# Performance work log

Hardware: AMD Instinct MI355X
Metric: run time of the kernel (lower is better)

Reference implementation:

```python
import jax, jax.numpy as jnp
import numpy as np

N, C, H, W, D = 4, 320, 16, 16, 16
POS_RATIO = 0.5


def setup_inputs() -> dict:
    key = jax.random.key(0)
    k1, k2, k3, k4 = jax.random.split(key, 4)
    q = jax.random.normal(k1, (N, C, H, W, D), jnp.float32)
    k = jax.random.normal(k2, (N, C, H, W, D), jnp.float32)

    def make_coord(kr):
        # crop boxes: upper-left corner in [0, 0.4), extent in [0.4, 0.6)
        start = jax.random.uniform(kr, (N, 3), jnp.float32) * 0.4
        size = 0.4 + jax.random.uniform(jax.random.fold_in(kr, 1), (N, 3), jnp.float32) * 0.2
        return jnp.concatenate([start, start + size], axis=1)  # (N, 6)

    coord_q = make_coord(k3)
    coord_k = make_coord(k4)
    return {"q": q, "k": k, "coord_q": coord_q, "coord_k": coord_k}


def _centers(coord, h, w, d):
    """coord: (N,6) -> centers (N, h*w*d, 3) of each voxel in global coords, and bin diag (N,)."""
    dims = jnp.array([h, w, d], jnp.float32)
    bin_sz = (coord[:, 3:6] - coord[:, 0:3]) / dims  # (N,3) = (bin_h, bin_w, bin_d)
    ax = jnp.arange(h, dtype=jnp.float32) + 0.5
    ay = jnp.arange(w, dtype=jnp.float32) + 0.5
    az = jnp.arange(d, dtype=jnp.float32) + 0.5
    grid = jnp.stack(jnp.meshgrid(ax, ay, az, indexing="ij"), axis=-1)  # (h,w,d,3)
    grid = grid.reshape(1, h * w * d, 3)
    centers = grid * bin_sz[:, None, :] + coord[:, None, 0:3]  # (N, L, 3)
    diag = jnp.sqrt(jnp.sum(bin_sz ** 2, axis=-1))  # (N,)
    return centers, diag


def reference(q, k, coord_q, coord_k):
    n, c, h, w, d = q.shape
    L = h * w * d
    qf = q.reshape(n, c, L)
    kf = k.reshape(n, c, L)

    cq, diag_q = _centers(coord_q, h, w, d)  # (N,L,3), (N,)
    ck, diag_k = _centers(coord_k, h, w, d)
    max_diag = jnp.maximum(diag_q, diag_k)[:, None, None]  # (N,1,1)

    def masked_loss(q_flat, centers_q):
        # pairwise center distance (N, L, L) -- sum of three squared diffs, no (N,L,L,3) stack
        d2 = ((centers_q[:, :, None, 0] - ck[:, None, :, 0]) ** 2
              + (centers_q[:, :, None, 1] - ck[:, None, :, 1]) ** 2
              + (centers_q[:, :, None, 2] - ck[:, None, :, 2]) ** 2)
        dist = jnp.sqrt(d2) / max_diag
        mask = jax.lax.stop_gradient((dist < POS_RATIO).astype(jnp.float32))
        logit = jnp.einsum("ncl,ncm->nlm", q_flat, kf)  # bmm(q^T, k)
        return jnp.sum(logit * mask, axis=(-2, -1)) / (jnp.sum(mask, axis=(-2, -1)) + 1e-6)

    loss = masked_loss(qf, cq)
    # anatomy branch: flip(q) and flipped q-centers along batch dim 0 (as in source flip(x, dim=0))
    loss_rev = masked_loss(jnp.flip(qf, axis=0), jnp.flip(cq, axis=0))
    return -2.0 * jnp.mean(loss) - 2.0 * jnp.mean(loss_rev)
```

## Files before the change

kernel.cpp:

```cpp
#include <hip/hip_runtime.h>

#define LVOX   4096
#define NCH    320
#define NCOMBO 8
#define RCAP   49152

struct Geo {
    float qs0, qs1, qs2, qo0, qo1, qo2;
    float ks0, ks1, ks2, ko0, ko1, ko2;
    float ik0, ik1, ik2;
    float T;
};

__device__ __forceinline__ Geo make_geo(const float* __restrict__ cq,
                                        const float* __restrict__ ck,
                                        int n, int qb) {
    Geo g;
    const float* qc = cq + qb * 6;
    const float* qn = cq + n * 6;
    const float* kc = ck + n * 6;
    g.qs0 = (qc[3] - qc[0]) * (1.f / 16.f); g.qo0 = qc[0];
    g.qs1 = (qc[4] - qc[1]) * (1.f / 16.f); g.qo1 = qc[1];
    g.qs2 = (qc[5] - qc[2]) * (1.f / 16.f); g.qo2 = qc[2];
    g.ks0 = (kc[3] - kc[0]) * (1.f / 16.f); g.ko0 = kc[0];
    g.ks1 = (kc[4] - kc[1]) * (1.f / 16.f); g.ko1 = kc[1];
    g.ks2 = (kc[5] - kc[2]) * (1.f / 16.f); g.ko2 = kc[2];
    g.ik0 = 1.f / g.ks0; g.ik1 = 1.f / g.ks1; g.ik2 = 1.f / g.ks2;
    float b0 = (qn[3] - qn[0]) * (1.f / 16.f);
    float b1 = (qn[4] - qn[1]) * (1.f / 16.f);
    float b2 = (qn[5] - qn[2]) * (1.f / 16.f);
    float dq = sqrtf(b0 * b0 + b1 * b1 + b2 * b2);
    float dk = sqrtf(g.ks0 * g.ks0 + g.ks1 * g.ks1 + g.ks2 * g.ks2);
    g.T = 0.5f * fmaxf(dq, dk);
    return g;
}

__device__ __forceinline__ void axrange(float c, float ko, float ik, float T,
                                        int& m0, int& m1) {
    float lo = (c - T - ko) * ik - 0.5f;
    float hi = (c + T - ko) * ik - 0.5f;
    m0 = max((int)ceilf(lo) - 1, 0);
    m1 = min((int)floorf(hi) + 1, 15);
}

__global__ void enum_runs(const float* __restrict__ coord_q,
                          const float* __restrict__ coord_k,
                          unsigned* __restrict__ pcnt,
                          unsigned* __restrict__ rcnt,
                          unsigned* __restrict__ runs, int cap) {
    int gid = blockIdx.x * 256 + threadIdx.x;
    int j = gid >> 12;
    int l = gid & 4095;
    int n = j & 3;
    int qb = (j & 4) ? (3 - n) : n;
    Geo g = make_geo(coord_q, coord_k, n, qb);

    int ix = l >> 8, iy = (l >> 4) & 15, iz = l & 15;
    float cx = (ix + 0.5f) * g.qs0 + g.qo0;
    float cy = (iy + 0.5f) * g.qs1 + g.qo1;
    float cz = (iz + 0.5f) * g.qs2 + g.qo2;
    int x0, x1, y0, y1, z0, z1;
    axrange(cx, g.ko0, g.ik0, g.T, x0, x1);
    axrange(cy, g.ko1, g.ik1, g.T, y0, y1);
    axrange(cz, g.ko2, g.ik2, g.T, z0, z1);

    int nh = 0, nr = 0;
    for (int x = x0; x <= x1; ++x) {
        float dx = cx - ((x + 0.5f) * g.ks0 + g.ko0);
        float dx2 = dx * dx;
        for (int y = y0; y <= y1; ++y) {
            float dy = cy - ((y + 0.5f) * g.ks1 + g.ko1);
            float dxy = dx2 + dy * dy;
            int zc = 0;
            for (int z = z0; z <= z1; ++z) {
                float dz = cz - ((z + 0.5f) * g.ks2 + g.ko2);
                if (sqrtf(dxy + dz * dz) < g.T) zc++;
            }
            if (zc) { nr++; nh += zc; }
        }
    }

    int lane = threadIdx.x & 63;
    int incl = nr;
#pragma unroll
    for (int off = 1; off < 64; off <<= 1) {
        int t = __shfl_up(incl, off, 64);
        if (lane >= off) incl += t;
    }
    int total = __shfl(incl, 63, 64);
    int base = 0;
    if (lane == 63) base = (int)atomicAdd(&rcnt[j], (unsigned)total);
    base = __shfl(base, 63, 64);
    int w = base + incl - nr;

    int hsum = nh;
#pragma unroll
    for (int off = 32; off; off >>= 1) hsum += __shfl_down(hsum, off, 64);
    if (lane == 0) atomicAdd(&pcnt[j], (unsigned)hsum);

    unsigned* out = runs + (size_t)j * (size_t)cap;
    for (int x = x0; x <= x1; ++x) {
        float dx = cx - ((x + 0.5f) * g.ks0 + g.ko0);
        float dx2 = dx * dx;
        for (int y = y0; y <= y1; ++y) {
            float dy = cy - ((y + 0.5f) * g.ks1 + g.ko1);
            float dxy = dx2 + dy * dy;
            int zf = -1, zc = 0;
            for (int z = z0; z <= z1; ++z) {
                float dz = cz - ((z + 0.5f) * g.ks2 + g.ko2);
                if (sqrtf(dxy + dz * dz) < g.T) { if (!zc) zf = z; zc++; }
            }
            if (zc) {
                if (w < cap)
                    out[w] = ((unsigned)l << 16)
                           | ((unsigned)((x << 8) | (y << 4) | zf) << 4)
                           | (unsigned)(zc - 1);
                w++;
            }
        }
    }
}

__global__ void __launch_bounds__(512) gather_runs(
        const float* __restrict__ q, const float* __restrict__ k,
        const unsigned* __restrict__ rcnt, const unsigned* __restrict__ runs,
        int cap, float* __restrict__ S) {
    __shared__ float qrow[LVOX];
    __shared__ float krow[LVOX + 16];
    __shared__ float sp[8];
    int j = blockIdx.x;
    int c = blockIdx.y;
    int n = j & 3;
    int qb = (j & 4) ? (3 - n) : n;
    const float* qsrc = q + ((size_t)(qb * NCH + c)) * LVOX;
    const float* ksrc = k + ((size_t)(n * NCH + c)) * LVOX;
    int t = threadIdx.x;

#pragma unroll
    for (int i = 0; i < 2; ++i) {
        int off = (t + 512 * i) * 4;
        *(float4*)&qrow[off] = *(const float4*)&qsrc[off];
        *(float4*)&krow[off] = *(const float4*)&ksrc[off];
    }
    if (t < 4) krow[LVOX + 4 * t] = 0.f;
    __syncthreads();

    unsigned cnt = rcnt[j];
    if (cnt > (unsigned)cap) cnt = (unsigned)cap;
    const unsigned* rl = runs + (size_t)j * (size_t)cap;

    float acc = 0.f;
    for (unsigned p = (unsigned)t * 4u; p < cnt; p += 512u * 4u) {
        uint4 r4 = *(const uint4*)&rl[p];
        unsigned rr[4] = {r4.x, r4.y, r4.z, r4.w};
#pragma unroll
        for (int e = 0; e < 4; ++e) {
            bool valid = (p + (unsigned)e) < cnt;
            unsigned pr = rr[e];
            int l  = (int)(pr >> 16) & 4095;
            int mb = (int)(pr >> 4) & 4095;
            int len = (int)(pr & 15u) + 1;
            float s = 0.f;
            for (int i = 0; i < len; ++i) s += krow[mb + i];
            acc += valid ? (qrow[l] * s) : 0.f;
        }
    }

#pragma unroll
    for (int off = 32; off; off >>= 1) acc += __shfl_down(acc, off, 64);
    int lane = t & 63;
    if (lane == 0) sp[t >> 6] = acc;
    __syncthreads();
    if (t == 0) {
        float v = 0.f;
#pragma unroll
        for (int i = 0; i < 8; ++i) v += sp[i];
        atomicAdd(&S[j], v);
    }
}

__global__ void finalize(const float* __restrict__ S,
                         const unsigned* __restrict__ pcnt,
                         float* __restrict__ out) {
    if (threadIdx.x == 0) {
        float t = 0.f;
#pragma unroll
        for (int j = 0; j < NCOMBO; ++j)
            t += S[j] / ((float)pcnt[j] + 1e-6f);
        out[0] = -0.5f * t;
    }
}

extern "C" void kernel_launch(void* const* d_in, const int* in_sizes, int n_in,
                              void* d_out, int out_size, void* d_ws, size_t ws_size,
                              hipStream_t stream) {
    const float* q       = (const float*)d_in[0];
    const float* k       = (const float*)d_in[1];
    const float* coord_q = (const float*)d_in[2];
    const float* coord_k = (const float*)d_in[3];
    float* out = (float*)d_out;

    float*    S    = (float*)d_ws;
    unsigned* pcnt = (unsigned*)d_ws + 8;
    unsigned* rcnt = (unsigned*)d_ws + 16;
    unsigned* runs = (unsigned*)((char*)d_ws + 128);

    size_t avail = (ws_size > 128) ? ((ws_size - 128) / 4) / NCOMBO : 4;
    avail &= ~(size_t)3;
    int cap = (int)((avail < (size_t)RCAP) ? avail : (size_t)RCAP);
    if (cap < 4) cap = 4;

    hipMemsetAsync(d_ws, 0, 128, stream);
    enum_runs<<<(NCOMBO * LVOX) / 256, 256, 0, stream>>>(coord_q, coord_k, pcnt, rcnt, runs, cap);
    gather_runs<<<dim3(NCOMBO, NCH), 512, 0, stream>>>(q, k, rcnt, runs, cap, S);
    finalize<<<1, 64, 0, stream>>>(S, pcnt, out);
}
```

Measured before the change: 139.1 us.

## Fuse combos per block, use prefix-summed k rows, drop atomics

The gather kernel now handles four batch/flip combinations per block (two q rows and two k rows shared across n and its mirrored partner), so each q/k channel row is loaded once instead of twice. K rows are stored in shared memory as per-(x,y) cell prefix sums with a padded stride, so each run sum becomes two shared-memory reads instead of a variable-length loop. Per-block partial sums go to a workspace array that finalize reduces, replacing global float atomics. The tradeoff is fewer blocks (640 vs 2560) with more shared memory each, which may reduce occupancy.

```diff
diff --git a/kernel.cpp b/kernel.cpp
--- a/kernel.cpp
+++ b/kernel.cpp
@@ -4,6 +4,11 @@
 #define NCH    320
 #define NCOMBO 8
 #define RCAP   49152
+#define PKSTR  17
+#define PKROW  (256 * PKSTR)
+#define NBLK   (2 * NCH)
+#define SPART_OFF 128
+#define RUNS_OFF  (SPART_OFF + NCOMBO * NBLK * 4)
 
 struct Geo {
     float qs0, qs1, qs2, qo0, qo1, qo2;
@@ -121,72 +126,114 @@
     }
 }
 
-__global__ void __launch_bounds__(512) gather_runs(
+__global__ void __launch_bounds__(512) gather_fused(
         const float* __restrict__ q, const float* __restrict__ k,
         const unsigned* __restrict__ rcnt, const unsigned* __restrict__ runs,
-        int cap, float* __restrict__ S) {
-    __shared__ float qrow[LVOX];
-    __shared__ float krow[LVOX + 16];
-    __shared__ float sp[8];
-    int j = blockIdx.x;
+        int cap, float* __restrict__ Spart) {
+    __shared__ float sh[2 * LVOX + 2 * PKROW + 32];
+    const int QA = 0, QB = LVOX, PK = 2 * LVOX, SR = 2 * LVOX + 2 * PKROW;
+
+    int g = blockIdx.x;
     int c = blockIdx.y;
-    int n = j & 3;
-    int qb = (j & 4) ? (3 - n) : n;
-    const float* qsrc = q + ((size_t)(qb * NCH + c)) * LVOX;
-    const float* ksrc = k + ((size_t)(n * NCH + c)) * LVOX;
+    int n0 = g ? 1 : 0;
+    int n1 = 3 - n0;
     int t = threadIdx.x;
 
+    const float* q0 = q + ((size_t)(n0 * NCH + c)) * LVOX;
+    const float* q1 = q + ((size_t)(n1 * NCH + c)) * LVOX;
 #pragma unroll
     for (int i = 0; i < 2; ++i) {
         int off = (t + 512 * i) * 4;
-        *(float4*)&qrow[off] = *(const float4*)&qsrc[off];
-        *(float4*)&krow[off] = *(const float4*)&ksrc[off];
-    }
-    if (t < 4) krow[LVOX + 4 * t] = 0.f;
+        *(float4*)&sh[QA + off] = *(const float4*)&q0[off];
+        *(float4*)&sh[QB + off] = *(const float4*)&q1[off];
+    }
+
+    {
+        int row = t >> 8;
+        int cl  = t & 255;
+        const float* ks = k + ((size_t)((row ? n1 : n0) * NCH + c)) * LVOX + cl * 16;
+        float4 v0 = *(const float4*)&ks[0];
+        float4 v1 = *(const float4*)&ks[4];
+        float4 v2 = *(const float4*)&ks[8];
+        float4 v3 = *(const float4*)&ks[12];
+        float vv[16] = {v0.x, v0.y, v0.z, v0.w, v1.x, v1.y, v1.z, v1.w,
+                        v2.x, v2.y, v2.z, v2.w, v3.x, v3.y, v3.z, v3.w};
+        float* dst = &sh[PK + row * PKROW + cl * PKSTR];
+        float e = 0.f;
+        dst[0] = 0.f;
+#pragma unroll
+        for (int i = 0; i < 16; ++i) { e += vv[i]; dst[i + 1] = e; }
+    }
     __syncthreads();
 
-    unsigned cnt = rcnt[j];
-    if (cnt > (unsigned)cap) cnt = (unsigned)cap;
-    const unsigned* rl = runs + (size_t)j * (size_t)cap;
-
-    float acc = 0.f;
-    for (unsigned p = (unsigned)t * 4u; p < cnt; p += 512u * 4u) {
-        uint4 r4 = *(const uint4*)&rl[p];
-        unsigned rr[4] = {r4.x, r4.y, r4.z, r4.w};
-#pragma unroll
-        for (int e = 0; e < 4; ++e) {
-            bool valid = (p + (unsigned)e) < cnt;
-            unsigned pr = rr[e];
-            int l  = (int)(pr >> 16) & 4095;
-            int mb = (int)(pr >> 4) & 4095;
-            int len = (int)(pr & 15u) + 1;
-            float s = 0.f;
-            for (int i = 0; i < len; ++i) s += krow[mb + i];
-            acc += valid ? (qrow[l] * s) : 0.f;
+    const int jl[4]   = {n0, n1, 4 + n0, 4 + n1};
+    const int qoff[4] = {QA, QB, QB, QA};
+    const int koff[4] = {PK, PK + PKROW, PK, PK + PKROW};
+    float accv[4];
+
+#pragma unroll
+    for (int ci = 0; ci < 4; ++ci) {
+        int j = jl[ci];
+        unsigned cnt = rcnt[j];
+        if (cnt > (unsigned)cap) cnt = (unsigned)cap;
+        const unsigned* rl = runs + (size_t)j * (size_t)cap;
+        int qb = qoff[ci], kb = koff[ci];
+        float acc = 0.f;
+        for (unsigned p = (unsigned)t * 4u; p < cnt; p += 512u * 4u) {
+            uint4 r4 = *(const uint4*)&rl[p];
+            unsigned rr[4] = {r4.x, r4.y, r4.z, r4.w};
+#pragma unroll
+            for (int e = 0; e < 4; ++e) {
+                bool valid = (p + (unsigned)e) < cnt;
+                unsigned pr = rr[e];
+                int l    = (int)(pr >> 16);
+                int cell = (int)((pr >> 8) & 255u);
+                int zf   = (int)((pr >> 4) & 15u);
+                int len  = (int)(pr & 15u) + 1;
+                float s = sh[kb + cell * PKSTR + zf + len] - sh[kb + cell * PKSTR + zf];
+                acc += valid ? sh[qb + l] * s : 0.f;
+            }
         }
-    }
-
-#pragma unroll
-    for (int off = 32; off; off >>= 1) acc += __shfl_down(acc, off, 64);
-    int lane = t & 63;
-    if (lane == 0) sp[t >> 6] = acc;
+        accv[ci] = acc;
+    }
+
+    int wv = t >> 6, lane = t & 63;
+#pragma unroll
+    for (int ci = 0; ci < 4; ++ci) {
+        float a = accv[ci];
+#pragma unroll
+        for (int off = 32; off; off >>= 1) a += __shfl_down(a, off, 64);
+        if (lane == 0) sh[SR + wv * 4 + ci] = a;
+    }
     __syncthreads();
-    if (t == 0) {
+    if (t < 4) {
         float v = 0.f;
 #pragma unroll
-        for (int i = 0; i < 8; ++i) v += sp[i];
-        atomicAdd(&S[j], v);
-    }
-}
-
-__global__ void finalize(const float* __restrict__ S,
+        for (int w = 0; w < 8; ++w) v += sh[SR + w * 4 + t];
+        Spart[(size_t)jl[t] * NBLK + (c * 2 + g)] = v;
+    }
+}
+
+__global__ void finalize(const float* __restrict__ Spart,
                          const unsigned* __restrict__ pcnt,
                          float* __restrict__ out) {
+    __shared__ float tj[NCOMBO];
+    int j = threadIdx.x >> 5;
+    int s = threadIdx.x & 31;
+    int nn = j & 3;
+    int gj = (nn == 1 || nn == 2) ? 1 : 0;
+    float v = 0.f;
+    for (int i = s; i < NCH; i += 32)
+        v += Spart[(size_t)j * NBLK + i * 2 + gj];
+#pragma unroll
+    for (int off = 16; off; off >>= 1) v += __shfl_down(v, off, 32);
+    if (s == 0) tj[j] = v;
+    __syncthreads();
     if (threadIdx.x == 0) {
         float t = 0.f;
 #pragma unroll
-        for (int j = 0; j < NCOMBO; ++j)
-            t += S[j] / ((float)pcnt[j] + 1e-6f);
+        for (int jj = 0; jj < NCOMBO; ++jj)
+            t += tj[jj] / ((float)pcnt[jj] + 1e-6f);
         out[0] = -0.5f * t;
     }
 }
@@ -200,18 +247,18 @@
     const float* coord_k = (const float*)d_in[3];
     float* out = (float*)d_out;
 
-    float*    S    = (float*)d_ws;
-    unsigned* pcnt = (unsigned*)d_ws + 8;
-    unsigned* rcnt = (unsigned*)d_ws + 16;
-    unsigned* runs = (unsigned*)((char*)d_ws + 128);
-
-    size_t avail = (ws_size > 128) ? ((ws_size - 128) / 4) / NCOMBO : 4;
+    unsigned* pcnt  = (unsigned*)d_ws;
+    unsigned* rcnt  = (unsigned*)d_ws + 8;
+    float*    Spart = (float*)((char*)d_ws + SPART_OFF);
+    unsigned* runs  = (unsigned*)((char*)d_ws + RUNS_OFF);
+
+    size_t avail = (ws_size > RUNS_OFF) ? ((ws_size - RUNS_OFF) / 4) / NCOMBO : 4;
     avail &= ~(size_t)3;
     int cap = (int)((avail < (size_t)RCAP) ? avail : (size_t)RCAP);
     if (cap < 4) cap = 4;
 
     hipMemsetAsync(d_ws, 0, 128, stream);
     enum_runs<<<(NCOMBO * LVOX) / 256, 256, 0, stream>>>(coord_q, coord_k, pcnt, rcnt, runs, cap);
-    gather_runs<<<dim3(NCOMBO, NCH), 512, 0, stream>>>(q, k, rcnt, runs, cap, S);
-    finalize<<<1, 64, 0, stream>>>(S, pcnt, out);
-}
+    gather_fused<<<dim3(2, NCH), 512, 0, stream>>>(q, k, rcnt, runs, cap, Spart);
+    finalize<<<1, 256, 0, stream>>>(Spart, pcnt, out);
+}
```

Measured after the change: 125.0 us. -10.1%, faster.
